# Kernel optimization log

Hardware: AMD Instinct MI355X
Metric: run time of the kernel (lower is better)

## Reference

```python
import jax, jax.numpy as jnp
import numpy as np

B, T, C, H = 4, 2048, 1024, 16
D = C // H  # head_dim = 64


def setup_inputs() -> dict:
    key = jax.random.key(0)
    ks = jax.random.split(key, 5)
    s = 0.02
    return {
        "x": jax.random.normal(ks[0], (B, T, C), dtype=jnp.float32),
        "w_qkv": jax.random.normal(ks[1], (C, 3 * C), dtype=jnp.float32) * s,
        "b_qkv": jnp.zeros((3 * C,), dtype=jnp.float32),
        "w_proj": jax.random.normal(ks[2], (C, C), dtype=jnp.float32) * s,
        "b_proj": jnp.zeros((C,), dtype=jnp.float32),
    }


def reference(x, w_qkv, b_qkv, w_proj, b_proj):
    Bx, Tx, Cx = x.shape
    qkv = x @ w_qkv + b_qkv                      # [B,T,3C]
    q, k, v = jnp.split(qkv, 3, axis=-1)
    # [B,T,C] -> [B,H,T,D]
    q = q.reshape(Bx, Tx, H, D).transpose(0, 2, 1, 3)
    k = k.reshape(Bx, Tx, H, D).transpose(0, 2, 1, 3)
    v = v.reshape(Bx, Tx, H, D).transpose(0, 2, 1, 3)
    scale = 1.0 / np.sqrt(D).astype(np.float32)
    attn = jnp.einsum('bhqd,bhkd->bhqk', q, k) * scale   # [B,H,T,T]
    causal = jnp.tril(jnp.ones((Tx, Tx), dtype=bool))
    attn = jnp.where(causal[None, None], attn, -jnp.inf)
    attn = jax.nn.softmax(attn, axis=-1)
    out = jnp.einsum('bhqk,bhkd->bhqd', attn, v)          # [B,H,T,D]
    out = out.transpose(0, 2, 1, 3).reshape(Bx, Tx, Cx)   # [B,T,C]
    return out @ w_proj + b_proj
```

## Files before the change

kernel.cpp:

```cpp
#include <hip/hip_runtime.h>
#include <hip/hip_bf16.h>
#include <math.h>

using bf16 = __hip_bfloat16;
typedef __bf16 bf16x8 __attribute__((ext_vector_type(8)));
typedef float  f32x4  __attribute__((ext_vector_type(4)));
typedef unsigned short ushort8 __attribute__((ext_vector_type(8)));
typedef unsigned uint4v __attribute__((ext_vector_type(4)));

#define DEV __device__ __forceinline__

DEV void gld_lds16(const void* g, void* l) {
    __builtin_amdgcn_global_load_lds((const __attribute__((address_space(1))) void*)g,
                                     (__attribute__((address_space(3))) void*)l,
                                     16, 0, 0);
}

__global__ __launch_bounds__(256) void prep(const float* __restrict__ x,
                                            bf16* __restrict__ xb,
                                            const float* __restrict__ w_qkv,
                                            bf16* __restrict__ wqkvT,
                                            const float* __restrict__ w_proj,
                                            bf16* __restrict__ wprojT) {
    __shared__ float tile[32][33];
    int blk = blockIdx.x;
    int tid = threadIdx.x;
    if (blk < 8192) {
        int i = blk * 256 + tid;
        float4 f = ((const float4*)x)[i];
        __align__(8) bf16 o[4] = {__float2bfloat16(f.x), __float2bfloat16(f.y),
                                  __float2bfloat16(f.z), __float2bfloat16(f.w)};
        ((uint64_t*)xb)[i] = *(const uint64_t*)o;
        return;
    }
    const float* in;
    bf16* out;
    int R, Cn, bx, by;
    if (blk < 11264) {
        int bid = blk - 8192;
        in = w_qkv; out = wqkvT; R = 1024; Cn = 3072;
        bx = (bid % 96) * 32; by = (bid / 96) * 32;
    } else {
        int bid = blk - 11264;
        in = w_proj; out = wprojT; R = 1024; Cn = 1024;
        bx = (bid % 32) * 32; by = (bid / 32) * 32;
    }
    int tx = tid & 31, ty = tid >> 5;
    for (int i = ty; i < 32; i += 8)
        tile[i][tx] = in[(size_t)(by + i) * Cn + bx + tx];
    __syncthreads();
    for (int i = ty; i < 32; i += 8)
        out[(size_t)(bx + i) * R + by + tx] = __float2bfloat16(tile[tx][i]);
}

__global__ __launch_bounds__(256) void gemm_qkv(const bf16* __restrict__ A,
                                                const bf16* __restrict__ Bt,
                                                const float* __restrict__ bias,
                                                bf16* __restrict__ qb,
                                                bf16* __restrict__ kb,
                                                bf16* __restrict__ vTb) {
    constexpr int K = 1024, T = 2048;
    constexpr float CS = 0.18033688f;
    __shared__ __align__(16) bf16 Al[128 * 32];
    __shared__ __align__(16) bf16 Bl[128 * 32];
    __shared__ __align__(16) bf16 Et[32 * 136];
    int tid = threadIdx.x;
    int lane = tid & 63, w = tid >> 6;
    int wm = w >> 1, wn = w & 1;
    int l15 = lane & 15, quad = lane >> 4;
    int m0 = blockIdx.x * 128, n0 = blockIdx.y * 128;
    int l3 = l15 & 3;

    f32x4 acc[4][4] = {};
    for (int k0 = 0; k0 < K; k0 += 32) {
        __syncthreads();
        for (int it = 0; it < 2; ++it) {
            int e = (it * 256 + tid) * 8;
            int r = e >> 5, cu = (e >> 3) & 3;
            int cs = ((cu ^ (r & 3)) << 3);
            gld_lds16(A  + (size_t)(m0 + r) * K + k0 + cs, &Al[e]);
            gld_lds16(Bt + (size_t)(n0 + r) * K + k0 + cs, &Bl[e]);
        }
        __syncthreads();
        bf16x8 af[4], bfr[4];
        for (int i = 0; i < 4; ++i)
            af[i] = *(const bf16x8*)&Al[(wm * 64 + i * 16 + l15) * 32 + ((quad ^ l3) << 3)];
        for (int j = 0; j < 4; ++j)
            bfr[j] = *(const bf16x8*)&Bl[(wn * 64 + j * 16 + l15) * 32 + ((quad ^ l3) << 3)];
        for (int i = 0; i < 4; ++i)
            for (int j = 0; j < 4; ++j)
                acc[i][j] = __builtin_amdgcn_mfma_f32_16x16x32_bf16(af[i], bfr[j], acc[i][j], 0, 0, 0);
    }

    int mode = (blockIdx.y < 8) ? 0 : (blockIdx.y < 16 ? 1 : 2);
    float bv[4];
    for (int j = 0; j < 4; ++j)
        bv[j] = bias[n0 + wn * 64 + j * 16 + l15];
    float scl = (mode == 0) ? CS : 1.0f;

    for (int i = 0; i < 4; ++i) {
        __syncthreads();
        for (int j = 0; j < 4; ++j)
            for (int v = 0; v < 4; ++v)
                Et[(wm * 16 + quad * 4 + v) * 136 + wn * 64 + j * 16 + l15] =
                    __float2bfloat16((acc[i][j][v] + bv[j]) * scl);
        __syncthreads();
        if (mode < 2) {
            int r = tid >> 3, cc = (tid & 7) * 16;
            int m = m0 + i * 16 + (r < 16 ? r : r + 48);
            int b = m >> 11, t = m & 2047;
            int n = (n0 & 1023) + cc;
            int h = n >> 6, d = n & 63;
            bf16* dst = (mode == 0 ? qb : kb) + (((size_t)(b * 16 + h)) * T + t) * 64 + d;
            ushort8 u0 = *(const ushort8*)&Et[r * 136 + cc];
            ushort8 u1 = *(const ushort8*)&Et[r * 136 + cc + 8];
            *(ushort8*)dst = u0;
            *(ushort8*)(dst + 8) = u1;
        } else {
            int run = tid >> 7, d = tid & 127;
            int t0 = m0 + i * 16 + run * 64;
            int b = t0 >> 11, tt = t0 & 2047;
            int n = (n0 & 1023) + d;
            int h = n >> 6, dd = n & 63;
            __align__(16) bf16 tmp[16];
            for (int jj = 0; jj < 16; ++jj)
                tmp[jj] = Et[(run * 16 + jj) * 136 + d];
            bf16* dst = vTb + (((size_t)(b * 16 + h)) * 64 + dd) * T + tt;
            *(ushort8*)dst = *(const ushort8*)tmp;
            *(ushort8*)(dst + 8) = *(const ushort8*)(tmp + 8);
        }
    }
}

__global__ __launch_bounds__(256, 4) void flash_attn(const bf16* __restrict__ qb,
                                                     const bf16* __restrict__ kbuf,
                                                     const bf16* __restrict__ vT,
                                                     bf16* __restrict__ ob) {
    constexpr int T = 2048;
    __shared__ __align__(16) bf16 Kl[2][64 * 64];
    __shared__ __align__(16) bf16 Vl[64 * 64];
    int tid = threadIdx.x;
    int lane = tid & 63, w = tid >> 6;
    int l15 = lane & 15, quad = lane >> 4;

    int g = blockIdx.x;
    int quarter = g >> 8;
    int j = (g >> 6) & 3;
    int bh = g & 63;
    int xq;
    switch (quarter) {
        case 0:  xq = 15 - j; break;
        case 1:  xq = 8 + j;  break;
        case 2:  xq = 4 + j;  break;
        default: xq = 3 - j;  break;
    }
    int q0 = xq << 7;
    const bf16* qbase = qb   + (size_t)bh * T * 64;
    const bf16* kbase = kbuf + (size_t)bh * T * 64;
    const bf16* vbase = vT   + (size_t)bh * 64 * T;

    int qg[2];
    bf16x8 qa[2][2];
#pragma unroll
    for (int s = 0; s < 2; ++s) {
        qg[s] = q0 + w * 32 + s * 16 + l15;
#pragma unroll
        for (int c = 0; c < 2; ++c)
            qa[s][c] = *(const bf16x8*)(qbase + (size_t)qg[s] * 64 + c * 32 + quad * 8);
    }

    bf16x8 ones;
#pragma unroll
    for (int i = 0; i < 8; ++i) ones[i] = (__bf16)1.0f;

    f32x4 O[2][4] = {};
    f32x4 O1[2] = {};
    int h7 = l15 & 7;

    int off0 = tid * 8, off1 = (256 + tid) * 8;
    int r0 = off0 >> 6, cb0 = (off0 >> 3) & 7;
    int r1 = off1 >> 6, cb1 = (off1 >> 3) & 7;
    int kc0 = (cb0 ^ (r0 & 7)) << 3, kc1 = (cb1 ^ (r1 & 7)) << 3;

    int nit = 2 * xq + 2;

    bf16x8 vr0 = *(const bf16x8*)(vbase + (size_t)r0 * T + kc0);
    bf16x8 vr1 = *(const bf16x8*)(vbase + (size_t)r1 * T + kc1);
    gld_lds16(kbase + (size_t)r0 * 64 + kc0, &Kl[0][off0]);
    gld_lds16(kbase + (size_t)r1 * 64 + kc1, &Kl[0][off1]);
    *(bf16x8*)&Vl[off0] = vr0;
    *(bf16x8*)&Vl[off1] = vr1;

    for (int t = 0; t < nit; ++t) {
        int cur = t & 1;
        __syncthreads();
        bool pre = (t + 1 < nit);
        if (pre) {
            int kb2 = (t + 1) << 6, nxt = cur ^ 1;
            vr0 = *(const bf16x8*)(vbase + (size_t)r0 * T + kb2 + kc0);
            vr1 = *(const bf16x8*)(vbase + (size_t)r1 * T + kb2 + kc1);
            gld_lds16(kbase + (size_t)(kb2 + r0) * 64 + kc0, &Kl[nxt][off0]);
            gld_lds16(kbase + (size_t)(kb2 + r1) * 64 + kc1, &Kl[nxt][off1]);
        }
        int kb = t << 6;
        bool maskt = (t >= nit - 2);

        unsigned Dq[2][4][2];
#pragma unroll
        for (int jn = 0; jn < 4; ++jn) {
            int row = jn * 16 + l15;
            bf16x8 a0 = *(const bf16x8*)&Kl[cur][row * 64 + ((quad ^ h7) << 3)];
            bf16x8 a1 = *(const bf16x8*)&Kl[cur][row * 64 + (((4 + quad) ^ h7) << 3)];
            f32x4 sa[2] = {};
            __builtin_amdgcn_s_setprio(1);
            sa[0] = __builtin_amdgcn_mfma_f32_16x16x32_bf16(a0, qa[0][0], sa[0], 0, 0, 0);
            sa[0] = __builtin_amdgcn_mfma_f32_16x16x32_bf16(a1, qa[0][1], sa[0], 0, 0, 0);
            sa[1] = __builtin_amdgcn_mfma_f32_16x16x32_bf16(a0, qa[1][0], sa[1], 0, 0, 0);
            sa[1] = __builtin_amdgcn_mfma_f32_16x16x32_bf16(a1, qa[1][1], sa[1], 0, 0, 0);
            __builtin_amdgcn_s_setprio(0);
#pragma unroll
            for (int s = 0; s < 2; ++s) {
                float p[4];
#pragma unroll
                for (int v = 0; v < 4; ++v) {
                    float e = __builtin_amdgcn_exp2f(sa[s][v]);
                    if (maskt) {
                        int key = kb + jn * 16 + quad * 4 + v;
                        e = (key <= qg[s]) ? e : 0.f;
                    }
                    p[v] = e;
                }
                unsigned lo, hi;
                asm("v_cvt_pk_bf16_f32 %0, %1, %2" : "=v"(lo) : "v"(p[0]), "v"(p[1]));
                asm("v_cvt_pk_bf16_f32 %0, %1, %2" : "=v"(hi) : "v"(p[2]), "v"(p[3]));
                Dq[s][jn][0] = lo;
                Dq[s][jn][1] = hi;
            }
        }

        bf16x8 pf[2][2];
#pragma unroll
        for (int s = 0; s < 2; ++s)
#pragma unroll
            for (int c = 0; c < 2; ++c) {
                uint4v wv;
#pragma unroll
                for (int h = 0; h < 2; ++h) {
                    unsigned X = Dq[s][2 * c][h];
                    unsigned Y = Dq[s][2 * c + 1][h];
                    asm("v_permlane32_swap_b32 %0, %1" : "+v"(X), "+v"(Y));
                    asm("v_permlane16_swap_b32 %0, %1" : "+v"(X), "+v"(Y));
                    wv[h]     = X;
                    wv[2 + h] = Y;
                }
                pf[s][c] = __builtin_bit_cast(bf16x8, wv);
            }

        __builtin_amdgcn_s_setprio(1);
#pragma unroll
        for (int s = 0; s < 2; ++s) {
            O1[s] = __builtin_amdgcn_mfma_f32_16x16x32_bf16(pf[s][0], ones, O1[s], 0, 0, 0);
            O1[s] = __builtin_amdgcn_mfma_f32_16x16x32_bf16(pf[s][1], ones, O1[s], 0, 0, 0);
        }
        __builtin_amdgcn_s_setprio(0);

#pragma unroll
        for (int jd = 0; jd < 4; ++jd) {
            int vrow = jd * 16 + l15;
            bf16x8 v0 = *(const bf16x8*)&Vl[vrow * 64 + ((quad ^ h7) << 3)];
            bf16x8 v1 = *(const bf16x8*)&Vl[vrow * 64 + (((4 + quad) ^ h7) << 3)];
            __builtin_amdgcn_s_setprio(1);
            O[0][jd] = __builtin_amdgcn_mfma_f32_16x16x32_bf16(pf[0][0], v0, O[0][jd], 0, 0, 0);
            O[0][jd] = __builtin_amdgcn_mfma_f32_16x16x32_bf16(pf[0][1], v1, O[0][jd], 0, 0, 0);
            O[1][jd] = __builtin_amdgcn_mfma_f32_16x16x32_bf16(pf[1][0], v0, O[1][jd], 0, 0, 0);
            O[1][jd] = __builtin_amdgcn_mfma_f32_16x16x32_bf16(pf[1][1], v1, O[1][jd], 0, 0, 0);
            __builtin_amdgcn_s_setprio(0);
        }

        __builtin_amdgcn_s_barrier();
        if (pre) {
            *(bf16x8*)&Vl[off0] = vr0;
            *(bf16x8*)&Vl[off1] = vr1;
        }
    }

    int b = bh >> 4, h = bh & 15;
#pragma unroll
    for (int s = 0; s < 2; ++s) {
        float linv[4];
#pragma unroll
        for (int v = 0; v < 4; ++v) linv[v] = 1.f / O1[s][v];
#pragma unroll
        for (int jd = 0; jd < 4; ++jd) {
#pragma unroll
            for (int v = 0; v < 4; ++v) {
                int qr = q0 + w * 32 + s * 16 + quad * 4 + v;
                ob[((size_t)(b * T + qr)) * 1024 + h * 64 + jd * 16 + l15] =
                    __float2bfloat16(O[s][jd][v] * linv[v]);
            }
        }
    }
}

__global__ __launch_bounds__(256) void gemm_proj(const bf16* __restrict__ A,
                                                 const bf16* __restrict__ Bt,
                                                 const float* __restrict__ bias,
                                                 float* __restrict__ out) {
    constexpr int K = 1024, N = 1024;
    __shared__ __align__(16) bf16 Al[128 * 32];
    __shared__ __align__(16) bf16 Bl[128 * 32];
    int tid = threadIdx.x;
    int lane = tid & 63, w = tid >> 6;
    int wm = w >> 1, wn = w & 1;
    int l15 = lane & 15, quad = lane >> 4;
    int m0 = blockIdx.x * 128, n0 = blockIdx.y * 128;
    int l3 = l15 & 3;

    f32x4 acc[4][4] = {};
    for (int k0 = 0; k0 < K; k0 += 32) {
        __syncthreads();
        for (int it = 0; it < 2; ++it) {
            int e = (it * 256 + tid) * 8;
            int r = e >> 5, cu = (e >> 3) & 3;
            int cs = ((cu ^ (r & 3)) << 3);
            gld_lds16(A  + (size_t)(m0 + r) * K + k0 + cs, &Al[e]);
            gld_lds16(Bt + (size_t)(n0 + r) * K + k0 + cs, &Bl[e]);
        }
        __syncthreads();
        bf16x8 af[4], bfr[4];
        for (int i = 0; i < 4; ++i)
            af[i] = *(const bf16x8*)&Al[(wm * 64 + i * 16 + l15) * 32 + ((quad ^ l3) << 3)];
        for (int j = 0; j < 4; ++j)
            bfr[j] = *(const bf16x8*)&Bl[(wn * 64 + j * 16 + l15) * 32 + ((quad ^ l3) << 3)];
        for (int i = 0; i < 4; ++i)
            for (int j = 0; j < 4; ++j)
                acc[i][j] = __builtin_amdgcn_mfma_f32_16x16x32_bf16(af[i], bfr[j], acc[i][j], 0, 0, 0);
    }
    for (int i = 0; i < 4; ++i) {
        int mbase = m0 + wm * 64 + i * 16 + quad * 4;
        for (int j = 0; j < 4; ++j) {
            int n = n0 + wn * 64 + j * 16 + l15;
            float bv = bias[n];
            for (int v = 0; v < 4; ++v)
                out[(size_t)(mbase + v) * N + n] = acc[i][j][v] + bv;
        }
    }
}

extern "C" void kernel_launch(void* const* d_in, const int* in_sizes, int n_in,
                              void* d_out, int out_size, void* d_ws, size_t ws_size,
                              hipStream_t stream) {
    (void)in_sizes; (void)n_in; (void)out_size; (void)ws_size;
    const float* x      = (const float*)d_in[0];
    const float* w_qkv  = (const float*)d_in[1];
    const float* b_qkv  = (const float*)d_in[2];
    const float* w_proj = (const float*)d_in[3];
    const float* b_proj = (const float*)d_in[4];
    float* out = (float*)d_out;

    char* ws = (char*)d_ws;
    bf16* xb     = (bf16*)(ws);
    bf16* wqkvT  = (bf16*)(ws + (16u << 20));
    bf16* wprojT = (bf16*)(ws + (22u << 20));
    bf16* qbuf   = (bf16*)(ws + (24u << 20));
    bf16* kbuf   = (bf16*)(ws + (40u << 20));
    bf16* vTb    = (bf16*)(ws + (72u << 20));
    bf16* ob     = (bf16*)(ws + (56u << 20));

    prep<<<12288, 256, 0, stream>>>(x, xb, w_qkv, wqkvT, w_proj, wprojT);
    gemm_qkv<<<dim3(64, 24), 256, 0, stream>>>(xb, wqkvT, b_qkv, qbuf, kbuf, vTb);
    flash_attn<<<1024, 256, 0, stream>>>(qbuf, kbuf, vTb, ob);
    gemm_proj<<<dim3(64, 8), 256, 0, stream>>>(ob, wprojT, b_proj, out);
}
```

Measured before the change: 238.8 us.

## Double-buffer LDS tiles in QKV and projection GEMM main loops

Both bf16 GEMM kernels switch from a single LDS tile pair to two buffers, processing two k-slices per loop iteration. The loads for the next slice are issued asynchronously via global_load_lds before the MFMA work on the current slice, so memory latency can overlap with compute. Per-thread address math is hoisted out of the loop. In exchange LDS use per block doubles, and the epilogue staging buffer now aliases the first tile buffer and spills into the second, which is safe only because a barrier comes first.

```diff
diff --git a/kernel.cpp b/kernel.cpp
--- a/kernel.cpp
+++ b/kernel.cpp
@@ -61,9 +61,8 @@
                                                 bf16* __restrict__ vTb) {
     constexpr int K = 1024, T = 2048;
     constexpr float CS = 0.18033688f;
-    __shared__ __align__(16) bf16 Al[128 * 32];
-    __shared__ __align__(16) bf16 Bl[128 * 32];
-    __shared__ __align__(16) bf16 Et[32 * 136];
+    __shared__ __align__(16) bf16 SM[4][128 * 32];
+    bf16* Et = &SM[0][0];
     int tid = threadIdx.x;
     int lane = tid & 63, w = tid >> 6;
     int wm = w >> 1, wn = w & 1;
@@ -71,25 +70,38 @@
     int m0 = blockIdx.x * 128, n0 = blockIdx.y * 128;
     int l3 = l15 & 3;
 
+    int e0 = tid * 8, e1 = (256 + tid) * 8;
+    int r0 = e0 >> 5, c0 = ((((e0 >> 3) & 3) ^ (r0 & 3)) << 3);
+    int r1 = e1 >> 5, c1 = ((((e1 >> 3) & 3) ^ (r1 & 3)) << 3);
+
     f32x4 acc[4][4] = {};
-    for (int k0 = 0; k0 < K; k0 += 32) {
-        __syncthreads();
-        for (int it = 0; it < 2; ++it) {
-            int e = (it * 256 + tid) * 8;
-            int r = e >> 5, cu = (e >> 3) & 3;
-            int cs = ((cu ^ (r & 3)) << 3);
-            gld_lds16(A  + (size_t)(m0 + r) * K + k0 + cs, &Al[e]);
-            gld_lds16(Bt + (size_t)(n0 + r) * K + k0 + cs, &Bl[e]);
-        }
-        __syncthreads();
+
+    auto STAGE = [&](int buf, int kc) {
+        gld_lds16(A  + (size_t)(m0 + r0) * K + kc + c0, &SM[buf][e0]);
+        gld_lds16(A  + (size_t)(m0 + r1) * K + kc + c1, &SM[buf][e1]);
+        gld_lds16(Bt + (size_t)(n0 + r0) * K + kc + c0, &SM[2 + buf][e0]);
+        gld_lds16(Bt + (size_t)(n0 + r1) * K + kc + c1, &SM[2 + buf][e1]);
+    };
+    auto COMP = [&](int buf) {
         bf16x8 af[4], bfr[4];
         for (int i = 0; i < 4; ++i)
-            af[i] = *(const bf16x8*)&Al[(wm * 64 + i * 16 + l15) * 32 + ((quad ^ l3) << 3)];
+            af[i] = *(const bf16x8*)&SM[buf][(wm * 64 + i * 16 + l15) * 32 + ((quad ^ l3) << 3)];
         for (int j = 0; j < 4; ++j)
-            bfr[j] = *(const bf16x8*)&Bl[(wn * 64 + j * 16 + l15) * 32 + ((quad ^ l3) << 3)];
+            bfr[j] = *(const bf16x8*)&SM[2 + buf][(wn * 64 + j * 16 + l15) * 32 + ((quad ^ l3) << 3)];
         for (int i = 0; i < 4; ++i)
             for (int j = 0; j < 4; ++j)
                 acc[i][j] = __builtin_amdgcn_mfma_f32_16x16x32_bf16(af[i], bfr[j], acc[i][j], 0, 0, 0);
+    };
+
+    STAGE(0, 0);
+    for (int t = 0; t < K / 64; ++t) {
+        int k0 = t * 64;
+        __syncthreads();
+        STAGE(1, k0 + 32);
+        COMP(0);
+        __syncthreads();
+        if (t + 1 < K / 64) STAGE(0, k0 + 64);
+        COMP(1);
     }
 
     int mode = (blockIdx.y < 8) ? 0 : (blockIdx.y < 16 ? 1 : 2);
@@ -307,8 +319,7 @@
                                                  const float* __restrict__ bias,
                                                  float* __restrict__ out) {
     constexpr int K = 1024, N = 1024;
-    __shared__ __align__(16) bf16 Al[128 * 32];
-    __shared__ __align__(16) bf16 Bl[128 * 32];
+    __shared__ __align__(16) bf16 SM[4][128 * 32];
     int tid = threadIdx.x;
     int lane = tid & 63, w = tid >> 6;
     int wm = w >> 1, wn = w & 1;
@@ -316,26 +327,40 @@
     int m0 = blockIdx.x * 128, n0 = blockIdx.y * 128;
     int l3 = l15 & 3;
 
+    int e0 = tid * 8, e1 = (256 + tid) * 8;
+    int r0 = e0 >> 5, c0 = ((((e0 >> 3) & 3) ^ (r0 & 3)) << 3);
+    int r1 = e1 >> 5, c1 = ((((e1 >> 3) & 3) ^ (r1 & 3)) << 3);
+
     f32x4 acc[4][4] = {};
-    for (int k0 = 0; k0 < K; k0 += 32) {
-        __syncthreads();
-        for (int it = 0; it < 2; ++it) {
-            int e = (it * 256 + tid) * 8;
-            int r = e >> 5, cu = (e >> 3) & 3;
-            int cs = ((cu ^ (r & 3)) << 3);
-            gld_lds16(A  + (size_t)(m0 + r) * K + k0 + cs, &Al[e]);
-            gld_lds16(Bt + (size_t)(n0 + r) * K + k0 + cs, &Bl[e]);
-        }
-        __syncthreads();
+
+    auto STAGE = [&](int buf, int kc) {
+        gld_lds16(A  + (size_t)(m0 + r0) * K + kc + c0, &SM[buf][e0]);
+        gld_lds16(A  + (size_t)(m0 + r1) * K + kc + c1, &SM[buf][e1]);
+        gld_lds16(Bt + (size_t)(n0 + r0) * K + kc + c0, &SM[2 + buf][e0]);
+        gld_lds16(Bt + (size_t)(n0 + r1) * K + kc + c1, &SM[2 + buf][e1]);
+    };
+    auto COMP = [&](int buf) {
         bf16x8 af[4], bfr[4];
         for (int i = 0; i < 4; ++i)
-            af[i] = *(const bf16x8*)&Al[(wm * 64 + i * 16 + l15) * 32 + ((quad ^ l3) << 3)];
+            af[i] = *(const bf16x8*)&SM[buf][(wm * 64 + i * 16 + l15) * 32 + ((quad ^ l3) << 3)];
         for (int j = 0; j < 4; ++j)
-            bfr[j] = *(const bf16x8*)&Bl[(wn * 64 + j * 16 + l15) * 32 + ((quad ^ l3) << 3)];
+            bfr[j] = *(const bf16x8*)&SM[2 + buf][(wn * 64 + j * 16 + l15) * 32 + ((quad ^ l3) << 3)];
         for (int i = 0; i < 4; ++i)
             for (int j = 0; j < 4; ++j)
                 acc[i][j] = __builtin_amdgcn_mfma_f32_16x16x32_bf16(af[i], bfr[j], acc[i][j], 0, 0, 0);
-    }
+    };
+
+    STAGE(0, 0);
+    for (int t = 0; t < K / 64; ++t) {
+        int k0 = t * 64;
+        __syncthreads();
+        STAGE(1, k0 + 32);
+        COMP(0);
+        __syncthreads();
+        if (t + 1 < K / 64) STAGE(0, k0 + 64);
+        COMP(1);
+    }
+
     for (int i = 0; i < 4; ++i) {
         int mbase = m0 + wm * 64 + i * 16 + quad * 4;
         for (int j = 0; j < 4; ++j) {
```

Result: no change. 237.5 us (-0.5%).
